# Kernel optimization log

Measured on AMD Instinct MI355X. Metric: run time of the kernel, lower is better.

## Reference

```python
import jax, jax.numpy as jnp
import numpy as np
import math

EMBED_DIM = 1024
NUM_HEADS = 16
HEAD_DIM = EMBED_DIM // NUM_HEADS
B, S = 4, 2048


def setup_inputs() -> dict:
    key = jax.random.key(0)
    ks = jax.random.split(key, 12)
    sc = 1.0 / math.sqrt(EMBED_DIM)
    inp = {
        'query': jax.random.normal(ks[0], (B, S, EMBED_DIM), jnp.float32),
        'key': jax.random.normal(ks[1], (B, S, EMBED_DIM), jnp.float32),
        'value': jax.random.normal(ks[2], (B, S, EMBED_DIM), jnp.float32),
        # causal mask: 1 = attend, 0 = masked (matches masked_fill(attn_mask == 0, -inf))
        'attn_mask': jnp.tril(jnp.ones((S, S), jnp.int32)),
        'Wq': jax.random.normal(ks[3], (EMBED_DIM, EMBED_DIM), jnp.float32) * sc,
        'bq': jax.random.normal(ks[4], (EMBED_DIM,), jnp.float32) * sc,
        'Wk': jax.random.normal(ks[5], (EMBED_DIM, EMBED_DIM), jnp.float32) * sc,
        'bk': jax.random.normal(ks[6], (EMBED_DIM,), jnp.float32) * sc,
        'Wv': jax.random.normal(ks[7], (EMBED_DIM, EMBED_DIM), jnp.float32) * sc,
        'bv': jax.random.normal(ks[8], (EMBED_DIM,), jnp.float32) * sc,
        'Wo': jax.random.normal(ks[9], (EMBED_DIM, EMBED_DIM), jnp.float32) * sc,
        'bo': jax.random.normal(ks[10], (EMBED_DIM,), jnp.float32) * sc,
    }
    return inp


def reference(query, key, value, attn_mask, Wq, bq, Wk, bk, Wv, bv, Wo, bo):
    b, s, _ = query.shape
    # torch nn.Linear: x @ W.T + b
    q = (query @ Wq.T + bq).reshape(b, s, NUM_HEADS, HEAD_DIM)
    k = (key @ Wk.T + bk).reshape(b, s, NUM_HEADS, HEAD_DIM)
    v = (value @ Wv.T + bv).reshape(b, s, NUM_HEADS, HEAD_DIM)
    scores = jnp.einsum('bqhd,bkhd->bhqk', q, k) / math.sqrt(HEAD_DIM)
    neg_inf = jnp.asarray(-jnp.inf, scores.dtype)
    scores = jnp.where(attn_mask[None, None, :, :] == 0, neg_inf, scores)
    attn = jax.nn.softmax(scores, axis=-1)
    # dropout is identity in eval mode
    out = jnp.einsum('bhqk,bkhd->bqhd', attn, v).reshape(b, s, EMBED_DIM)
    return out @ Wo.T + bo
```

## Files before the change

kernel.cpp:

```cpp
#include <hip/hip_runtime.h>
#include <math.h>


#define EMBED 1024
#define SEQ   2048
#define NH    16
#define HD    64
#define QSCALE 0.18033688011112042f

typedef __attribute__((ext_vector_type(4))) float f32x4;
typedef __attribute__((ext_vector_type(8))) short s16x8;
typedef __attribute__((ext_vector_type(4))) short s16x4;
typedef __attribute__((ext_vector_type(4))) unsigned int u32x4;
typedef __attribute__((ext_vector_type(2))) unsigned int u32x2;

#define GLDS16(gp, lp) __builtin_amdgcn_global_load_lds( \
    (const __attribute__((address_space(1))) void*)(gp), \
    (__attribute__((address_space(3))) void*)(lp), 16, 0, 0)

__device__ __forceinline__ unsigned short f2bf(float f) {
    unsigned int u = __builtin_bit_cast(unsigned int, f);
    u += 0x7fffu + ((u >> 16) & 1u);
    return (unsigned short)(u >> 16);
}
__device__ __forceinline__ unsigned int pkbf(float lo, float hi) {
    return __builtin_amdgcn_perm(__builtin_bit_cast(unsigned int, hi),
                                 __builtin_bit_cast(unsigned int, lo),
                                 0x07060302u);
}

struct CvtArgs { const float* s[7]; unsigned short* d[7]; int n4[7]; };
__global__ void cvt_all(CvtArgs ca)
{
    const int t = blockIdx.y;
    const float* in = ca.s[t];
    unsigned short* out = ca.d[t];
    const int n4 = ca.n4[t];
    const int stride = gridDim.x * 256;
    for (int i = blockIdx.x * 256 + threadIdx.x; i < n4; i += stride) {
        f32x4 v = *(const f32x4*)(in + (size_t)i * 4);
        s16x4 p;
        p[0] = (short)f2bf(v[0]); p[1] = (short)f2bf(v[1]);
        p[2] = (short)f2bf(v[2]); p[3] = (short)f2bf(v[3]);
        *(s16x4*)(out + (size_t)i * 4) = p;
    }
}

struct ProjArgs {
    const unsigned short* X[3];
    const unsigned short* W[3];
    const float* Bz[3];
    unsigned short* Oz[3];
};
__global__ void __launch_bounds__(256, 4)
gemm_qkv(ProjArgs pa)
{
    __shared__ unsigned short Ab[128 * 64];
    __shared__ unsigned short Bb[128 * 64];
    const int z = blockIdx.z;
    const unsigned short* Xb = pa.X[z];
    const unsigned short* Wb = pa.W[z];
    const float* bias = pa.Bz[z];
    unsigned short* Out = pa.Oz[z];
    const float scale = (z == 0) ? QSCALE : 1.0f;
    const int tid = threadIdx.x, lane = tid & 63, wv = tid >> 6;
    const int g = lane >> 4, c = lane & 15;
    const int wx = wv & 1, wy = wv >> 1;
    const int bm0 = blockIdx.x * 128, bn0 = blockIdx.y * 128;

    f32x4 acc[4][4];
#pragma unroll
    for (int i = 0; i < 4; ++i)
#pragma unroll
        for (int n = 0; n < 4; ++n) acc[i][n] = f32x4{0.f, 0.f, 0.f, 0.f};

    for (int k0 = 0; k0 < EMBED; k0 += 64) {
        __syncthreads();
#pragma unroll
        for (int cc = 0; cc < 4; ++cc) {
            int li = cc * 256 + tid;
            int row = li >> 3, ch = (li & 7) ^ (row & 7);
            GLDS16(Xb + (size_t)(bm0 + row) * EMBED + k0 + ch * 8,
                   Ab + cc * 2048 + wv * 512);
        }
#pragma unroll
        for (int cc = 0; cc < 4; ++cc) {
            int li = cc * 256 + tid;
            int row = li >> 3, ch = (li & 7) ^ (row & 7);
            GLDS16(Wb + (size_t)(bn0 + row) * EMBED + k0 + ch * 8,
                   Bb + cc * 2048 + wv * 512);
        }
        __syncthreads();
#pragma unroll
        for (int ks = 0; ks < 2; ++ks) {
            const int ib = ((ks * 4 + g) ^ (c & 7)) * 8;
            s16x8 af[4], bfr[4];
#pragma unroll
            for (int i = 0; i < 4; ++i)
                af[i] = *(const s16x8*)(&Ab[(wy * 64 + i * 16 + c) * 64 + ib]);
#pragma unroll
            for (int n = 0; n < 4; ++n)
                bfr[n] = *(const s16x8*)(&Bb[(wx * 64 + n * 16 + c) * 64 + ib]);
#pragma unroll
            for (int i = 0; i < 4; ++i)
#pragma unroll
                for (int n = 0; n < 4; ++n)
                    acc[i][n] = __builtin_amdgcn_mfma_f32_16x16x32_bf16(af[i], bfr[n], acc[i][n], 0, 0, 0);
        }
    }
    if (z < 2) {
#pragma unroll
        for (int i = 0; i < 4; ++i) {
            int m0 = bm0 + wy * 64 + i * 16 + g * 4;
            int bb = m0 >> 11, s0 = m0 & 2047;
#pragma unroll
            for (int n = 0; n < 4; ++n) {
                int ncol = bn0 + wx * 64 + n * 16 + c;
                float bv = bias[ncol];
                int hh = ncol >> 6, dd = ncol & 63;
                size_t base = (((size_t)bb * NH + hh) * SEQ + s0) * HD + dd;
#pragma unroll
                for (int r = 0; r < 4; ++r)
                    Out[base + (size_t)r * HD] = f2bf((acc[i][n][r] + bv) * scale);
            }
        }
    } else {
#pragma unroll
        for (int i = 0; i < 4; ++i) {
            int m0 = bm0 + wy * 64 + i * 16 + g * 4;
            int bb = m0 >> 11, s0 = m0 & 2047;
#pragma unroll
            for (int n = 0; n < 4; ++n) {
                int ncol = bn0 + wx * 64 + n * 16 + c;
                float bv = bias[ncol];
                int hh = ncol >> 6, dd = ncol & 63;
                s16x4 pk;
#pragma unroll
                for (int r = 0; r < 4; ++r) pk[r] = (short)f2bf(acc[i][n][r] + bv);
                *(s16x4*)(&Out[(((size_t)bb * NH + hh) * HD + dd) * SEQ + s0]) = pk;
            }
        }
    }
}

__global__ void __launch_bounds__(256, 4)
gemm_out(const unsigned short* __restrict__ Xb, const unsigned short* __restrict__ Wb,
         const float* __restrict__ bias, float* __restrict__ Out)
{
    __shared__ unsigned short Ab[128 * 64];
    __shared__ unsigned short Bb[128 * 64];
    const int tid = threadIdx.x;
    const int lane = tid & 63, wv = tid >> 6;
    const int g = lane >> 4, c = lane & 15;
    const int wx = wv & 1, wy = wv >> 1;
    const int bm0 = blockIdx.x * 128, bn0 = blockIdx.y * 128;

    f32x4 acc[4][4];
#pragma unroll
    for (int i = 0; i < 4; ++i)
#pragma unroll
        for (int n = 0; n < 4; ++n) acc[i][n] = f32x4{0.f, 0.f, 0.f, 0.f};

    for (int k0 = 0; k0 < EMBED; k0 += 64) {
        __syncthreads();
#pragma unroll
        for (int cc = 0; cc < 4; ++cc) {
            int li = cc * 256 + tid;
            int row = li >> 3, ch = (li & 7) ^ (row & 7);
            GLDS16(Xb + (size_t)(bm0 + row) * EMBED + k0 + ch * 8,
                   Ab + cc * 2048 + wv * 512);
        }
#pragma unroll
        for (int cc = 0; cc < 4; ++cc) {
            int li = cc * 256 + tid;
            int row = li >> 3, ch = (li & 7) ^ (row & 7);
            GLDS16(Wb + (size_t)(bn0 + row) * EMBED + k0 + ch * 8,
                   Bb + cc * 2048 + wv * 512);
        }
        __syncthreads();
#pragma unroll
        for (int ks = 0; ks < 2; ++ks) {
            const int ib = ((ks * 4 + g) ^ (c & 7)) * 8;
            s16x8 af[4], bfr[4];
#pragma unroll
            for (int i = 0; i < 4; ++i)
                af[i] = *(const s16x8*)(&Ab[(wy * 64 + i * 16 + c) * 64 + ib]);
#pragma unroll
            for (int n = 0; n < 4; ++n)
                bfr[n] = *(const s16x8*)(&Bb[(wx * 64 + n * 16 + c) * 64 + ib]);
#pragma unroll
            for (int i = 0; i < 4; ++i)
#pragma unroll
                for (int n = 0; n < 4; ++n)
                    acc[i][n] = __builtin_amdgcn_mfma_f32_16x16x32_bf16(af[i], bfr[n], acc[i][n], 0, 0, 0);
        }
    }
#pragma unroll
    for (int i = 0; i < 4; ++i) {
#pragma unroll
        for (int n = 0; n < 4; ++n) {
            int ncol = bn0 + wx * 64 + n * 16 + c;
            float bv = bias[ncol];
#pragma unroll
            for (int r = 0; r < 4; ++r) {
                int m = bm0 + wy * 64 + i * 16 + g * 4 + r;
                Out[(size_t)m * EMBED + ncol] = acc[i][n][r] + bv;
            }
        }
    }
}

__global__ void __launch_bounds__(512, 4)
attn_fwd(const unsigned short* __restrict__ Qb, const unsigned short* __restrict__ Kb,
         const unsigned short* __restrict__ Vg, unsigned short* __restrict__ Ob)
{
    __shared__ unsigned short Kt[2][64 * 64];
    __shared__ unsigned short Vt[2][64 * 64];
    __shared__ unsigned int   Pb[8][16 * 36];
    const int tid = threadIdx.x, lane = tid & 63, wv = tid >> 6;
    const int g = lane >> 4, c = lane & 15;
    const int wq = wv >> 2, wr = wv & 3;
    const int h = blockIdx.x, b = blockIdx.y;
    const int jj = 15 - blockIdx.z;
    const size_t bh = (size_t)b * NH + h;
    const unsigned short* K0 = Kb + bh * SEQ * HD;
    const unsigned short* V0 = Vg + bh * HD * SEQ;
    unsigned int* Pw = &Pb[wv][0];
    const int x0 = (g ^ (c & 7)) * 8;
    const int x1 = ((4 + g) ^ (c & 7)) * 8;
    const int srow = tid >> 3, sch = (tid & 7) ^ (srow & 7);
    const int kr = srow * HD + sch * 8;
    const int vr = srow * SEQ + sch * 8;

    const int qt = 2 * jj + wq;
    const int kmax = 2 * jj + 1;
    const unsigned short* Qp = Qb + (bh * SEQ + qt * 64 + wr * 16) * HD;
    s16x8 qf0 = *(const s16x8*)(Qp + c * HD + g * 8);
    s16x8 qf1 = *(const s16x8*)(Qp + c * HD + 32 + g * 8);
    f32x4 o[4];
#pragma unroll
    for (int dt = 0; dt < 4; ++dt) o[dt] = f32x4{0.f, 0.f, 0.f, 0.f};
    float m_run = -INFINITY, l_run = 0.f;

    {
        GLDS16(K0 + kr, &Kt[0][0] + wv * 512);
        GLDS16(V0 + vr, &Vt[0][0] + wv * 512);
    }

    for (int kt = 0; kt <= kmax; ++kt) {
        __syncthreads();
        const int cur = kt & 1;
        if (kt < kmax) {
            GLDS16(K0 + (size_t)(kt + 1) * 64 * HD + kr, &Kt[cur ^ 1][0] + wv * 512);
            GLDS16(V0 + (kt + 1) * 64 + vr, &Vt[cur ^ 1][0] + wv * 512);
        }
        if (kt > qt) continue;
        const unsigned short* Kc = &Kt[cur][0];
        const unsigned short* Vc = &Vt[cur][0];

        const int ntmax = (kt == qt) ? wr : 3;
        f32x4 sc[4];
        __builtin_amdgcn_s_setprio(1);
#pragma unroll
        for (int nt = 0; nt < 4; ++nt) {
            if (nt <= ntmax) {
                f32x4 a = f32x4{0.f, 0.f, 0.f, 0.f};
                s16x8 kf0 = *(const s16x8*)(&Kc[(nt * 16 + c) * 64 + x0]);
                s16x8 kf1 = *(const s16x8*)(&Kc[(nt * 16 + c) * 64 + x1]);
                a = __builtin_amdgcn_mfma_f32_16x16x32_bf16(kf0, qf0, a, 0, 0, 0);
                a = __builtin_amdgcn_mfma_f32_16x16x32_bf16(kf1, qf1, a, 0, 0, 0);
                sc[nt] = a;
            } else {
                sc[nt] = f32x4{-INFINITY, -INFINITY, -INFINITY, -INFINITY};
            }
        }
        __builtin_amdgcn_s_setprio(0);
        if (kt == qt) {
#pragma unroll
            for (int nt = 0; nt < 4; ++nt)
#pragma unroll
                for (int r = 0; r < 4; ++r)
                    if (nt * 16 + g * 4 + r > wr * 16 + c) sc[nt][r] = -INFINITY;
        }
        float mloc = -INFINITY;
#pragma unroll
        for (int nt = 0; nt < 4; ++nt)
            mloc = fmaxf(mloc, fmaxf(fmaxf(sc[nt][0], sc[nt][1]),
                                     fmaxf(sc[nt][2], sc[nt][3])));
        mloc = fmaxf(mloc, __shfl_xor(mloc, 16));
        mloc = fmaxf(mloc, __shfl_xor(mloc, 32));
        if (__any(mloc > m_run + 8.0f)) {
            float mnew = fmaxf(m_run, mloc);
            float alpha = __builtin_amdgcn_exp2f(m_run - mnew);
            m_run = mnew;
            l_run *= alpha;
            float av[4];
#pragma unroll
            for (int r = 0; r < 4; ++r) av[r] = __shfl(alpha, g * 4 + r, 16);
#pragma unroll
            for (int dt = 0; dt < 4; ++dt)
#pragma unroll
                for (int r = 0; r < 4; ++r) o[dt][r] *= av[r];
        }
        float rs = 0.f;
#pragma unroll
        for (int nt = 0; nt < 4; ++nt)
#pragma unroll
            for (int r = 0; r < 4; ++r) {
                float p = __builtin_amdgcn_exp2f(sc[nt][r] - m_run);
                sc[nt][r] = p;
                rs += p;
            }
        rs += __shfl_xor(rs, 16);
        rs += __shfl_xor(rs, 32);
        l_run += rs;
#pragma unroll
        for (int nt = 0; nt < 4; ++nt) {
            u32x2 w;
            w[0] = pkbf(sc[nt][0], sc[nt][1]);
            w[1] = pkbf(sc[nt][2], sc[nt][3]);
            *(u32x2*)(&Pw[c * 36 + nt * 8 + g * 2]) = w;
        }
        __builtin_amdgcn_s_setprio(1);
#pragma unroll
        for (int kc = 0; kc < 2; ++kc) {
            s16x8 pf = *(const s16x8*)(&Pw[c * 36 + kc * 16 + g * 4]);
            const int xv = kc ? x1 : x0;
#pragma unroll
            for (int dt = 0; dt < 4; ++dt) {
                s16x8 vf = *(const s16x8*)(&Vc[(dt * 16 + c) * 64 + xv]);
                o[dt] = __builtin_amdgcn_mfma_f32_16x16x32_bf16(pf, vf, o[dt], 0, 0, 0);
            }
        }
        __builtin_amdgcn_s_setprio(0);
    }
    float linv = 1.0f / l_run;
    float lv[4];
#pragma unroll
    for (int r = 0; r < 4; ++r) lv[r] = __shfl(linv, g * 4 + r, 16);
#pragma unroll
    for (int r = 0; r < 4; ++r) {
        int sr = qt * 64 + wr * 16 + g * 4 + r;
        size_t base = ((size_t)b * SEQ + sr) * EMBED + h * HD;
#pragma unroll
        for (int dt = 0; dt < 4; ++dt)
            Ob[base + dt * 16 + c] = f2bf(o[dt][r] * lv[r]);
    }
}

extern "C" void kernel_launch(void* const* d_in, const int* in_sizes, int n_in,
                              void* d_out, int out_size, void* d_ws, size_t ws_size,
                              hipStream_t stream)
{
    (void)in_sizes; (void)n_in; (void)out_size; (void)ws_size;
    const float* Xq = (const float*)d_in[0];
    const float* Xk = (const float*)d_in[1];
    const float* Xv = (const float*)d_in[2];
    const float* Wq = (const float*)d_in[4];
    const float* bq = (const float*)d_in[5];
    const float* Wk = (const float*)d_in[6];
    const float* bk = (const float*)d_in[7];
    const float* Wv = (const float*)d_in[8];
    const float* bv = (const float*)d_in[9];
    const float* Wo = (const float*)d_in[10];
    const float* bo = (const float*)d_in[11];
    float* Out = (float*)d_out;

    unsigned short* ws = (unsigned short*)d_ws;
    unsigned short* wqb = ws;
    unsigned short* wkb = wqb + 1048576;
    unsigned short* wvb = wkb + 1048576;
    unsigned short* wob = wvb + 1048576;
    unsigned short* xqb = wob + 1048576;
    unsigned short* xkb = xqb + 8388608;
    unsigned short* xvb = xkb + 8388608;
    unsigned short* Qb  = xvb + 8388608;
    unsigned short* Kb  = Qb + 8388608;
    unsigned short* Vb  = Kb + 8388608;
    unsigned short* Ax  = xqb;

    CvtArgs ca;
    ca.s[0] = Wq; ca.s[1] = Wk; ca.s[2] = Wv; ca.s[3] = Wo;
    ca.s[4] = Xq; ca.s[5] = Xk; ca.s[6] = Xv;
    ca.d[0] = wqb; ca.d[1] = wkb; ca.d[2] = wvb; ca.d[3] = wob;
    ca.d[4] = xqb; ca.d[5] = xkb; ca.d[6] = xvb;
    ca.n4[0] = ca.n4[1] = ca.n4[2] = ca.n4[3] = 262144;
    ca.n4[4] = ca.n4[5] = ca.n4[6] = 2097152;
    cvt_all<<<dim3(2048, 7), 256, 0, stream>>>(ca);

    ProjArgs pa;
    pa.X[0] = xqb; pa.X[1] = xkb; pa.X[2] = xvb;
    pa.W[0] = wqb; pa.W[1] = wkb; pa.W[2] = wvb;
    pa.Bz[0] = bq; pa.Bz[1] = bk; pa.Bz[2] = bv;
    pa.Oz[0] = Qb; pa.Oz[1] = Kb; pa.Oz[2] = Vb;
    gemm_qkv<<<dim3(64, 8, 3), 256, 0, stream>>>(pa);

    attn_fwd<<<dim3(NH, 4, 16), 512, 0, stream>>>(Qb, Kb, Vb, Ax);

    gemm_out<<<dim3(64, 8), 256, 0, stream>>>(Ax, wob, bo, Out);
}
```

Baseline: 316.6 us.

## Rewrite attention with 32x32 MFMA tiles and register-permuted P operand

```diff
diff --git a/kernel.cpp b/kernel.cpp
--- a/kernel.cpp
+++ b/kernel.cpp
@@ -9,6 +9,7 @@
 #define QSCALE 0.18033688011112042f
 
 typedef __attribute__((ext_vector_type(4))) float f32x4;
+typedef __attribute__((ext_vector_type(16))) float f32x16;
 typedef __attribute__((ext_vector_type(8))) short s16x8;
 typedef __attribute__((ext_vector_type(4))) short s16x4;
 typedef __attribute__((ext_vector_type(4))) unsigned int u32x4;
@@ -210,141 +211,145 @@
     }
 }
 
-__global__ void __launch_bounds__(512, 4)
+__global__ void __launch_bounds__(256, 4)
 attn_fwd(const unsigned short* __restrict__ Qb, const unsigned short* __restrict__ Kb,
          const unsigned short* __restrict__ Vg, unsigned short* __restrict__ Ob)
 {
     __shared__ unsigned short Kt[2][64 * 64];
     __shared__ unsigned short Vt[2][64 * 64];
-    __shared__ unsigned int   Pb[8][16 * 36];
     const int tid = threadIdx.x, lane = tid & 63, wv = tid >> 6;
-    const int g = lane >> 4, c = lane & 15;
-    const int wq = wv >> 2, wr = wv & 3;
+    const int c31 = lane & 31, a = lane >> 5;
     const int h = blockIdx.x, b = blockIdx.y;
     const int jj = 15 - blockIdx.z;
     const size_t bh = (size_t)b * NH + h;
     const unsigned short* K0 = Kb + bh * SEQ * HD;
     const unsigned short* V0 = Vg + bh * HD * SEQ;
-    unsigned int* Pw = &Pb[wv][0];
-    const int x0 = (g ^ (c & 7)) * 8;
-    const int x1 = ((4 + g) ^ (c & 7)) * 8;
-    const int srow = tid >> 3, sch = (tid & 7) ^ (srow & 7);
-    const int kr = srow * HD + sch * 8;
-    const int vr = srow * SEQ + sch * 8;
-
-    const int qt = 2 * jj + wq;
+    const int li1 = 256 + tid;
+    const int kr0 = (tid >> 3) * HD + (((tid & 7) ^ ((tid >> 3) & 7)) << 3);
+    const int kr1 = (li1 >> 3) * HD + (((li1 & 7) ^ ((li1 >> 3) & 7)) << 3);
+    const int vr0 = (tid >> 3) * SEQ + (((tid & 7) ^ ((tid >> 3) & 7)) << 3);
+    const int vr1 = (li1 >> 3) * SEQ + (((li1 & 7) ^ ((li1 >> 3) & 7)) << 3);
+
+    const int qw = jj * 128 + wv * 32;
     const int kmax = 2 * jj + 1;
-    const unsigned short* Qp = Qb + (bh * SEQ + qt * 64 + wr * 16) * HD;
-    s16x8 qf0 = *(const s16x8*)(Qp + c * HD + g * 8);
-    s16x8 qf1 = *(const s16x8*)(Qp + c * HD + 32 + g * 8);
-    f32x4 o[4];
-#pragma unroll
-    for (int dt = 0; dt < 4; ++dt) o[dt] = f32x4{0.f, 0.f, 0.f, 0.f};
+    const int sw7 = (c31 & 7);
+    const int pidx = (lane ^ 32) << 2;
+
+    const unsigned short* Qp = Qb + (bh * SEQ + qw + c31) * HD + a * 8;
+    s16x8 qf[4];
+#pragma unroll
+    for (int dwin = 0; dwin < 4; ++dwin)
+        qf[dwin] = *(const s16x8*)(Qp + dwin * 16);
+
+    f32x16 o[2];
+#pragma unroll
+    for (int r = 0; r < 16; ++r) { o[0][r] = 0.f; o[1][r] = 0.f; }
     float m_run = -INFINITY, l_run = 0.f;
 
     {
-        GLDS16(K0 + kr, &Kt[0][0] + wv * 512);
-        GLDS16(V0 + vr, &Vt[0][0] + wv * 512);
+        GLDS16(K0 + kr0, &Kt[0][0] + wv * 512);
+        GLDS16(K0 + kr1, &Kt[0][2048] + wv * 512);
+        GLDS16(V0 + vr0, &Vt[0][0] + wv * 512);
+        GLDS16(V0 + vr1, &Vt[0][2048] + wv * 512);
     }
 
     for (int kt = 0; kt <= kmax; ++kt) {
         __syncthreads();
         const int cur = kt & 1;
         if (kt < kmax) {
-            GLDS16(K0 + (size_t)(kt + 1) * 64 * HD + kr, &Kt[cur ^ 1][0] + wv * 512);
-            GLDS16(V0 + (kt + 1) * 64 + vr, &Vt[cur ^ 1][0] + wv * 512);
-        }
-        if (kt > qt) continue;
+            const unsigned short* Kg = K0 + (size_t)(kt + 1) * 64 * HD;
+            GLDS16(Kg + kr0, &Kt[cur ^ 1][0] + wv * 512);
+            GLDS16(Kg + kr1, &Kt[cur ^ 1][2048] + wv * 512);
+            const unsigned short* Vp = V0 + (kt + 1) * 64;
+            GLDS16(Vp + vr0, &Vt[cur ^ 1][0] + wv * 512);
+            GLDS16(Vp + vr1, &Vt[cur ^ 1][2048] + wv * 512);
+        }
+        if (kt * 64 > qw) continue;
         const unsigned short* Kc = &Kt[cur][0];
         const unsigned short* Vc = &Vt[cur][0];
 
-        const int ntmax = (kt == qt) ? wr : 3;
-        f32x4 sc[4];
-        __builtin_amdgcn_s_setprio(1);
-#pragma unroll
-        for (int nt = 0; nt < 4; ++nt) {
-            if (nt <= ntmax) {
-                f32x4 a = f32x4{0.f, 0.f, 0.f, 0.f};
-                s16x8 kf0 = *(const s16x8*)(&Kc[(nt * 16 + c) * 64 + x0]);
-                s16x8 kf1 = *(const s16x8*)(&Kc[(nt * 16 + c) * 64 + x1]);
-                a = __builtin_amdgcn_mfma_f32_16x16x32_bf16(kf0, qf0, a, 0, 0, 0);
-                a = __builtin_amdgcn_mfma_f32_16x16x32_bf16(kf1, qf1, a, 0, 0, 0);
-                sc[nt] = a;
-            } else {
-                sc[nt] = f32x4{-INFINITY, -INFINITY, -INFINITY, -INFINITY};
-            }
-        }
-        __builtin_amdgcn_s_setprio(0);
-        if (kt == qt) {
-#pragma unroll
-            for (int nt = 0; nt < 4; ++nt)
-#pragma unroll
-                for (int r = 0; r < 4; ++r)
-                    if (nt * 16 + g * 4 + r > wr * 16 + c) sc[nt][r] = -INFINITY;
-        }
-        float mloc = -INFINITY;
-#pragma unroll
-        for (int nt = 0; nt < 4; ++nt)
-            mloc = fmaxf(mloc, fmaxf(fmaxf(sc[nt][0], sc[nt][1]),
-                                     fmaxf(sc[nt][2], sc[nt][3])));
-        mloc = fmaxf(mloc, __shfl_xor(mloc, 16));
-        mloc = fmaxf(mloc, __shfl_xor(mloc, 32));
-        if (__any(mloc > m_run + 8.0f)) {
-            float mnew = fmaxf(m_run, mloc);
-            float alpha = __builtin_amdgcn_exp2f(m_run - mnew);
-            m_run = mnew;
-            l_run *= alpha;
-            float av[4];
-#pragma unroll
-            for (int r = 0; r < 4; ++r) av[r] = __shfl(alpha, g * 4 + r, 16);
-#pragma unroll
-            for (int dt = 0; dt < 4; ++dt)
-#pragma unroll
-                for (int r = 0; r < 4; ++r) o[dt][r] *= av[r];
-        }
-        float rs = 0.f;
-#pragma unroll
-        for (int nt = 0; nt < 4; ++nt)
-#pragma unroll
-            for (int r = 0; r < 4; ++r) {
-                float p = __builtin_amdgcn_exp2f(sc[nt][r] - m_run);
-                sc[nt][r] = p;
+#pragma unroll
+        for (int ks = 0; ks < 2; ++ks) {
+            const int kb = kt * 64 + ks * 32;
+            if (kb > qw) break;
+            f32x16 s;
+#pragma unroll
+            for (int r = 0; r < 16; ++r) s[r] = 0.f;
+            __builtin_amdgcn_s_setprio(1);
+#pragma unroll
+            for (int dwin = 0; dwin < 4; ++dwin) {
+                s16x8 kf = *(const s16x8*)(&Kc[(ks * 32 + c31) * 64 +
+                                               (((dwin * 2 + a) ^ sw7) << 3)]);
+                s = __builtin_amdgcn_mfma_f32_32x32x16_bf16(kf, qf[dwin], s, 0, 0, 0);
+            }
+            __builtin_amdgcn_s_setprio(0);
+            if (kb == qw) {
+#pragma unroll
+                for (int r = 0; r < 16; ++r) {
+                    int kr = (r & 3) + 8 * (r >> 2) + 4 * a;
+                    if (kr > c31) s[r] = -INFINITY;
+                }
+            }
+            float mloc = s[0];
+#pragma unroll
+            for (int r = 1; r < 16; ++r) mloc = fmaxf(mloc, s[r]);
+            mloc = fmaxf(mloc, __shfl_xor(mloc, 32));
+            if (__any(mloc > m_run + 8.0f)) {
+                float mnew = fmaxf(m_run, mloc);
+                float alpha = __builtin_amdgcn_exp2f(m_run - mnew);
+                m_run = mnew;
+                l_run *= alpha;
+#pragma unroll
+                for (int r = 0; r < 16; ++r) { o[0][r] *= alpha; o[1][r] *= alpha; }
+            }
+            float rs = 0.f;
+#pragma unroll
+            for (int r = 0; r < 16; ++r) {
+                float p = __builtin_amdgcn_exp2f(s[r] - m_run);
+                s[r] = p;
                 rs += p;
             }
-        rs += __shfl_xor(rs, 16);
-        rs += __shfl_xor(rs, 32);
-        l_run += rs;
-#pragma unroll
-        for (int nt = 0; nt < 4; ++nt) {
-            u32x2 w;
-            w[0] = pkbf(sc[nt][0], sc[nt][1]);
-            w[1] = pkbf(sc[nt][2], sc[nt][3]);
-            *(u32x2*)(&Pw[c * 36 + nt * 8 + g * 2]) = w;
-        }
-        __builtin_amdgcn_s_setprio(1);
-#pragma unroll
-        for (int kc = 0; kc < 2; ++kc) {
-            s16x8 pf = *(const s16x8*)(&Pw[c * 36 + kc * 16 + g * 4]);
-            const int xv = kc ? x1 : x0;
-#pragma unroll
-            for (int dt = 0; dt < 4; ++dt) {
-                s16x8 vf = *(const s16x8*)(&Vc[(dt * 16 + c) * 64 + xv]);
-                o[dt] = __builtin_amdgcn_mfma_f32_16x16x32_bf16(pf, vf, o[dt], 0, 0, 0);
-            }
-        }
-        __builtin_amdgcn_s_setprio(0);
+            rs += __shfl_xor(rs, 32);
+            l_run += rs;
+#pragma unroll
+            for (int win = 0; win < 2; ++win) {
+                unsigned int X0 = pkbf(s[8 * win + 0], s[8 * win + 1]);
+                unsigned int X1 = pkbf(s[8 * win + 2], s[8 * win + 3]);
+                unsigned int Y0 = pkbf(s[8 * win + 4], s[8 * win + 5]);
+                unsigned int Y1 = pkbf(s[8 * win + 6], s[8 * win + 7]);
+                unsigned int bX0 = (unsigned int)__builtin_amdgcn_ds_bpermute(pidx, (int)X0);
+                unsigned int bX1 = (unsigned int)__builtin_amdgcn_ds_bpermute(pidx, (int)X1);
+                unsigned int bY0 = (unsigned int)__builtin_amdgcn_ds_bpermute(pidx, (int)Y0);
+                unsigned int bY1 = (unsigned int)__builtin_amdgcn_ds_bpermute(pidx, (int)Y1);
+                u32x4 pd;
+                pd[0] = a ? bY0 : X0;
+                pd[1] = a ? bY1 : X1;
+                pd[2] = a ? Y0 : bX0;
+                pd[3] = a ? Y1 : bX1;
+                s16x8 pf = __builtin_bit_cast(s16x8, pd);
+                __builtin_amdgcn_s_setprio(1);
+#pragma unroll
+                for (int dh = 0; dh < 2; ++dh) {
+                    s16x8 vf = *(const s16x8*)(&Vc[(dh * 32 + c31) * 64 +
+                                                   (((ks * 4 + win * 2 + a) ^ sw7) << 3)]);
+                    o[dh] = __builtin_amdgcn_mfma_f32_32x32x16_bf16(vf, pf, o[dh], 0, 0, 0);
+                }
+                __builtin_amdgcn_s_setprio(0);
+            }
+        }
     }
     float linv = 1.0f / l_run;
-    float lv[4];
-#pragma unroll
-    for (int r = 0; r < 4; ++r) lv[r] = __shfl(linv, g * 4 + r, 16);
-#pragma unroll
-    for (int r = 0; r < 4; ++r) {
-        int sr = qt * 64 + wr * 16 + g * 4 + r;
-        size_t base = ((size_t)b * SEQ + sr) * EMBED + h * HD;
-#pragma unroll
-        for (int dt = 0; dt < 4; ++dt)
-            Ob[base + dt * 16 + c] = f2bf(o[dt][r] * lv[r]);
+    size_t rowbase = ((size_t)b * SEQ + qw + c31) * EMBED + h * HD;
+#pragma unroll
+    for (int dh = 0; dh < 2; ++dh) {
+#pragma unroll
+        for (int rq = 0; rq < 4; ++rq) {
+            s16x4 pk;
+#pragma unroll
+            for (int j = 0; j < 4; ++j)
+                pk[j] = (short)f2bf(o[dh][rq * 4 + j] * linv);
+            *(s16x4*)(&Ob[rowbase + dh * 32 + rq * 8 + a * 4]) = pk;
+        }
     }
 }
 
@@ -395,7 +400,7 @@
     pa.Oz[0] = Qb; pa.Oz[1] = Kb; pa.Oz[2] = Vb;
     gemm_qkv<<<dim3(64, 8, 3), 256, 0, stream>>>(pa);
 
-    attn_fwd<<<dim3(NH, 4, 16), 512, 0, stream>>>(Qb, Kb, Vb, Ax);
+    attn_fwd<<<dim3(NH, 4, 16), 256, 0, stream>>>(Qb, Kb, Vb, Ax);
 
     gemm_out<<<dim3(64, 8), 256, 0, stream>>>(Ax, wob, bo, Out);
 }
```

Result: no change. 318.2 us (+0.5%).
